# Kernel optimization log

Hardware: AMD Instinct MI355X
Metric: run time of the kernel (lower is better)

Reference implementation:

```python
import jax, jax.numpy as jnp
import numpy as np

D_MODEL = 1024
NUM_HEADS = 16
D_K = D_MODEL // NUM_HEADS
LN_EPS = 1e-5


def setup_inputs() -> dict:
    key = jax.random.key(0)
    ks = jax.random.split(key, 16)
    B, SQ, SK = 2, 2048, 2048
    s = 1.0 / np.sqrt(D_MODEL)
    inp = {
        "query": jax.random.normal(ks[0], (B, SQ, D_MODEL), jnp.float32),
        "key": jax.random.normal(ks[1], (B, SK, D_MODEL), jnp.float32),
        "value": jax.random.normal(ks[2], (B, SK, D_MODEL), jnp.float32),
        "mask": jax.random.randint(ks[3], (B, SQ, SK), 0, 2, jnp.int32),
        "w_q": jax.random.normal(ks[4], (D_MODEL, D_MODEL), jnp.float32) * s,
        "b_q": jnp.zeros((D_MODEL,), jnp.float32),
        "w_k": jax.random.normal(ks[5], (D_MODEL, D_MODEL), jnp.float32) * s,
        "b_k": jnp.zeros((D_MODEL,), jnp.float32),
        "w_v": jax.random.normal(ks[6], (D_MODEL, D_MODEL), jnp.float32) * s,
        "b_v": jnp.zeros((D_MODEL,), jnp.float32),
        "w_o": jax.random.normal(ks[7], (D_MODEL, D_MODEL), jnp.float32) * s,
        "b_o": jnp.zeros((D_MODEL,), jnp.float32),
        "ln_gamma": jnp.ones((D_MODEL,), jnp.float32),
        "ln_beta": jnp.zeros((D_MODEL,), jnp.float32),
    }
    return inp


def _split_heads(x):
    B, S, _ = x.shape
    return x.reshape(B, S, NUM_HEADS, D_K).transpose(0, 2, 1, 3)  # [B,H,S,Dk]


def reference(query, key, value, mask, w_q, b_q, w_k, b_k, w_v, b_v, w_o, b_o, ln_gamma, ln_beta):
    residual = query
    # torch Linear: y = x @ W.T + b
    Q = _split_heads(jnp.einsum('bsd,ed->bse', query, w_q) + b_q)
    K = _split_heads(jnp.einsum('bsd,ed->bse', key, w_k) + b_k)
    V = _split_heads(jnp.einsum('bsd,ed->bse', value, w_v) + b_v)
    scores = jnp.einsum('bhqd,bhkd->bhqk', Q, K) / jnp.sqrt(jnp.float32(D_K))
    scores = jnp.where(mask[:, None, :, :] == 0, jnp.float32(-1e9), scores)
    attn = jax.nn.softmax(scores, axis=-1)
    # dropout: eval mode (identity)
    ctx = jnp.einsum('bhqk,bhkd->bhqd', attn, V)
    B, H, SQ, Dk = ctx.shape
    ctx = ctx.transpose(0, 2, 1, 3).reshape(B, SQ, D_MODEL)
    out = jnp.einsum('bsd,ed->bse', ctx, w_o) + b_o + residual
    mu = jnp.mean(out, axis=-1, keepdims=True)
    var = jnp.mean(jnp.square(out - mu), axis=-1, keepdims=True)
    out = (out - mu) * jax.lax.rsqrt(var + LN_EPS) * ln_gamma + ln_beta
    return out
```

## Files before the change

kernel.cpp:

```cpp
#include <hip/hip_runtime.h>

typedef unsigned short u16;
typedef __attribute__((ext_vector_type(8))) short bf16x8;
typedef __attribute__((ext_vector_type(4))) float f32x4;

#define LOG2E 1.4426950408889634f
#define QSCALE (LOG2E / 8.0f)
#define PSTR 144

__device__ __forceinline__ u16 f2bf(float f) {
  union { float f; unsigned u; } v; v.f = f;
  unsigned r = v.u + 0x7fffu + ((v.u >> 16) & 1u);
  return (u16)(r >> 16);
}

__device__ __forceinline__ void gload_lds16(const void* g, void* l) {
  __builtin_amdgcn_global_load_lds(
      (const __attribute__((address_space(1))) unsigned int*)(unsigned long long)g,
      (__attribute__((address_space(3))) unsigned int*)(unsigned int)(unsigned long long)l,
      16, 0, 0);
}

__global__ __launch_bounds__(256) void prep_kernel(
    const float* __restrict__ q, const float* __restrict__ k, const float* __restrict__ v,
    const float* __restrict__ wq, const float* __restrict__ wk, const float* __restrict__ wv,
    const float* __restrict__ wo, const int* __restrict__ mask,
    u16* __restrict__ Xq, u16* __restrict__ Xk, u16* __restrict__ Xv,
    u16* __restrict__ Wq, u16* __restrict__ Wk, u16* __restrict__ Wv, u16* __restrict__ Wo,
    unsigned long long* __restrict__ Mp) {
  const int bx = blockIdx.x;
  if (bx < 16384) {
    const float* src; u16* dst; float sc; int idx;
    if (bx < 12288) {
      int seg = bx >> 12;
      idx = (bx & 4095) * 256 + threadIdx.x;
      src = seg == 0 ? q : (seg == 1 ? k : v);
      dst = seg == 0 ? Xq : (seg == 1 ? Xk : Xv);
      sc = 1.f;
    } else {
      int t = bx - 12288, seg = t >> 10;
      idx = (t & 1023) * 256 + threadIdx.x;
      src = seg == 0 ? wq : (seg == 1 ? wk : (seg == 2 ? wv : wo));
      dst = seg == 0 ? Wq : (seg == 1 ? Wk : (seg == 2 ? Wv : Wo));
      sc = seg == 0 ? QSCALE : 1.f;
    }
    float4 x = ((const float4*)src)[idx];
    ushort4 o;
    o.x = f2bf(x.x * sc); o.y = f2bf(x.y * sc);
    o.z = f2bf(x.z * sc); o.w = f2bf(x.w * sc);
    ((ushort4*)dst)[idx] = o;
  } else {
    int gw = (((bx - 16384) * 256) + threadIdx.x) >> 6;
    int lane = threadIdx.x & 63;
    for (int w = gw; w < 131072; w += 4096) {
      int m = mask[(size_t)w * 64 + lane];
      unsigned long long b = __ballot(m != 0);
      if (lane == 0) Mp[w] = b;
    }
  }
}

__global__ __launch_bounds__(256, 2) void gemm_kernel(
    const u16* __restrict__ Xq, const u16* __restrict__ Xk, const u16* __restrict__ Xv,
    const u16* __restrict__ Wq, const u16* __restrict__ Wk, const u16* __restrict__ Wv,
    const u16* __restrict__ Wo, const u16* __restrict__ Ctx,
    const float* __restrict__ bq, const float* __restrict__ bk, const float* __restrict__ bv,
    const float* __restrict__ bo, const float* __restrict__ resid,
    u16* __restrict__ Qd, u16* __restrict__ Kd, u16* __restrict__ Vtd, float* __restrict__ outp,
    int mode_base) {
  __shared__ __align__(16) u16 As[4096];
  __shared__ __align__(16) u16 Bs[4096];
  const int mode = mode_base + blockIdx.z;
  const int tid = threadIdx.x;
  const int wid = tid >> 6, l = tid & 63, quad = l >> 4, ln = l & 15;
  const int wm = wid >> 1, wn = wid & 1;

  const u16 *A, *B; const float* bias;
  if (mode == 0)      { A = Wq; B = Xq;  bias = bq; }
  else if (mode == 1) { A = Wk; B = Xk;  bias = bk; }
  else if (mode == 2) { A = Xv; B = Wv;  bias = bv; }
  else                { A = Wo; B = Ctx; bias = bo; }
  int mBase, nBase;
  if (mode == 2) { mBase = blockIdx.x * 128; nBase = blockIdx.y * 128; }
  else           { mBase = blockIdx.y * 128; nBase = blockIdx.x * 128; }

  const u16* Ag = A + (size_t)mBase * 1024;
  const u16* Bg = B + (size_t)nBase * 1024;

  f32x4 acc[4][4] = {};

  for (int k0 = 0; k0 < 1024; k0 += 32) {
    if (k0) __syncthreads();
    {
      int i0 = tid, i1 = tid + 256;
      gload_lds16(Ag + (size_t)(i0 & 127) * 1024 + k0 + (i0 >> 7) * 8, &As[i0 * 8]);
      gload_lds16(Ag + (size_t)(i1 & 127) * 1024 + k0 + (i1 >> 7) * 8, &As[i1 * 8]);
      gload_lds16(Bg + (size_t)(i0 & 127) * 1024 + k0 + (i0 >> 7) * 8, &Bs[i0 * 8]);
      gload_lds16(Bg + (size_t)(i1 & 127) * 1024 + k0 + (i1 >> 7) * 8, &Bs[i1 * 8]);
    }
    __syncthreads();
    bf16x8 af[4], bf[4];
#pragma unroll
    for (int i = 0; i < 4; ++i)
      af[i] = *(const bf16x8*)&As[(quad * 128 + wm * 64 + i * 16 + ln) * 8];
#pragma unroll
    for (int j = 0; j < 4; ++j)
      bf[j] = *(const bf16x8*)&Bs[(quad * 128 + wn * 64 + j * 16 + ln) * 8];
#pragma unroll
    for (int i = 0; i < 4; ++i)
#pragma unroll
      for (int j = 0; j < 4; ++j)
        acc[i][j] = __builtin_amdgcn_mfma_f32_16x16x32_bf16(af[i], bf[j], acc[i][j], 0, 0, 0);
  }

  const float bscale = (mode == 0) ? QSCALE : 1.0f;
#pragma unroll
  for (int i = 0; i < 4; ++i) {
    int m4 = mBase + wm * 64 + i * 16 + quad * 4;
#pragma unroll
    for (int j = 0; j < 4; ++j) {
      int n = nBase + wn * 64 + j * 16 + ln;
      f32x4 v = acc[i][j];
      if (mode <= 1) {
        float4 bb = *(const float4*)(bias + m4);
        int h = m4 >> 6, d = m4 & 63;
        int b = n >> 11, s = n & 2047;
        u16* dst = (mode == 0 ? Qd : Kd) + (((size_t)(b * 16 + h) * 2048 + s) * 64 + d);
        ushort4 o;
        o.x = f2bf(v[0] + bb.x * bscale); o.y = f2bf(v[1] + bb.y * bscale);
        o.z = f2bf(v[2] + bb.z * bscale); o.w = f2bf(v[3] + bb.w * bscale);
        *(ushort4*)dst = o;
      } else if (mode == 2) {
        float bb = bias[n];
        int h = n >> 6, d = n & 63;
        int b = m4 >> 11, s = m4 & 2047;
        u16* dst = Vtd + (((size_t)(b * 16 + h) * 64 + d) * 2048 + s);
        ushort4 o;
        o.x = f2bf(v[0] + bb); o.y = f2bf(v[1] + bb);
        o.z = f2bf(v[2] + bb); o.w = f2bf(v[3] + bb);
        *(ushort4*)dst = o;
      } else {
        float4 bb = *(const float4*)(bias + m4);
        float4 rr = *(const float4*)(resid + (size_t)n * 1024 + m4);
        float4 o;
        o.x = v[0] + bb.x + rr.x; o.y = v[1] + bb.y + rr.y;
        o.z = v[2] + bb.z + rr.z; o.w = v[3] + bb.w + rr.w;
        *(float4*)(outp + (size_t)n * 1024 + m4) = o;
      }
    }
  }
}

__global__ __launch_bounds__(256, 2) void attn_kernel(
    const u16* __restrict__ Qg, const u16* __restrict__ Kg, const u16* __restrict__ Vtg,
    const unsigned* __restrict__ Mp, u16* __restrict__ ctx) {
  __shared__ __align__(16) u16 UN[18432];
  __shared__ __align__(16) u16 Vs[8192];
  const int tid = threadIdx.x;
  const int wid = tid >> 6, l = tid & 63, quad = l >> 4, ln = l & 15;
  const int q4 = quad * 4;
  const int bh = blockIdx.y, b = bh >> 4, h = bh & 15;
  const int qBase = blockIdx.x * 128;
  const int wq = wid * 32;

  bf16x8 qf[2][2];
#pragma unroll
  for (int qt = 0; qt < 2; ++qt)
#pragma unroll
    for (int kc = 0; kc < 2; ++kc)
      qf[qt][kc] = *(const bf16x8*)(Qg + (((size_t)bh * 2048 + qBase + wq + qt * 16 + ln) * 64 +
                                          kc * 32 + quad * 8));

  f32x4 oacc[2][4] = {};
  f32x4 lsum[2] = {};
  const bf16x8 vone = {(short)0x3F80, (short)0x3F80, (short)0x3F80, (short)0x3F80,
                       (short)0x3F80, (short)0x3F80, (short)0x3F80, (short)0x3F80};

  const unsigned* mrow[2];
  mrow[0] = Mp + ((size_t)b * 2048 + qBase + wq + ln) * 64;
  mrow[1] = mrow[0] + 16 * 64;

  for (int it = 0; it < 16; ++it) {
    const int kvB = it * 128;
    __syncthreads();
#pragma unroll
    for (int r = 0; r < 4; ++r) {
      int c = r * 256 + tid;
      gload_lds16(Kg + (((size_t)bh * 2048 + kvB + (c & 127)) * 64 + (c >> 7) * 8), &UN[c * 8]);
    }
#pragma unroll
    for (int r = 0; r < 4; ++r) {
      int c = r * 256 + tid;
      gload_lds16(Vtg + (((size_t)bh * 64 + (c & 63)) * 2048 + kvB + (c >> 6) * 8), &Vs[c * 8]);
    }
    __syncthreads();

    f32x4 s[8][2];
#pragma unroll
    for (int mt = 0; mt < 8; ++mt) {
      bf16x8 k0 = *(const bf16x8*)&UN[((0 + quad) * 128 + mt * 16 + ln) * 8];
      bf16x8 k1 = *(const bf16x8*)&UN[((4 + quad) * 128 + mt * 16 + ln) * 8];
#pragma unroll
      for (int qt = 0; qt < 2; ++qt) {
        f32x4 z = {0.f, 0.f, 0.f, 0.f};
        z = __builtin_amdgcn_mfma_f32_16x16x32_bf16(k0, qf[qt][0], z, 0, 0, 0);
        s[mt][qt] = __builtin_amdgcn_mfma_f32_16x16x32_bf16(k1, qf[qt][1], z, 0, 0, 0);
      }
    }

    unsigned ww[2][4];
    {
      uint4 m0 = *(const uint4*)(mrow[0] + it * 4);
      uint4 m1 = *(const uint4*)(mrow[1] + it * 4);
      ww[0][0] = m0.x; ww[0][1] = m0.y; ww[0][2] = m0.z; ww[0][3] = m0.w;
      ww[1][0] = m1.x; ww[1][1] = m1.y; ww[1][2] = m1.z; ww[1][3] = m1.w;
    }
    uint2 pk[8][2];
#pragma unroll
    for (int qt = 0; qt < 2; ++qt)
#pragma unroll
      for (int mt = 0; mt < 8; ++mt) {
        unsigned nib = (ww[qt][mt >> 1] >> ((mt & 1) * 16 + q4)) & 0xFu;
        float p0 = __builtin_amdgcn_exp2f((nib & 1u) ? s[mt][qt][0] : -1e30f);
        float p1 = __builtin_amdgcn_exp2f((nib & 2u) ? s[mt][qt][1] : -1e30f);
        float p2 = __builtin_amdgcn_exp2f((nib & 4u) ? s[mt][qt][2] : -1e30f);
        float p3 = __builtin_amdgcn_exp2f((nib & 8u) ? s[mt][qt][3] : -1e30f);
        pk[mt][qt].x = __builtin_amdgcn_perm(__float_as_uint(p1) + 0x8000u,
                                             __float_as_uint(p0) + 0x8000u, 0x07060302u);
        pk[mt][qt].y = __builtin_amdgcn_perm(__float_as_uint(p3) + 0x8000u,
                                             __float_as_uint(p2) + 0x8000u, 0x07060302u);
      }

    __syncthreads();
#pragma unroll
    for (int qt = 0; qt < 2; ++qt) {
      int qrow = wq + qt * 16 + ln;
#pragma unroll
      for (int mt = 0; mt < 8; ++mt)
        *(uint2*)&UN[qrow * PSTR + mt * 16 + q4] = pk[mt][qt];
    }
    __syncthreads();

#pragma unroll
    for (int kc2 = 0; kc2 < 4; ++kc2) {
      bf16x8 aP[2];
#pragma unroll
      for (int qt = 0; qt < 2; ++qt)
        aP[qt] = *(const bf16x8*)&UN[(wq + qt * 16 + ln) * PSTR + kc2 * 32 + quad * 8];
#pragma unroll
      for (int nt = 0; nt < 4; ++nt) {
        bf16x8 bV = *(const bf16x8*)&Vs[((kc2 * 4 + quad) * 64 + nt * 16 + ln) * 8];
#pragma unroll
        for (int qt = 0; qt < 2; ++qt)
          oacc[qt][nt] = __builtin_amdgcn_mfma_f32_16x16x32_bf16(aP[qt], bV, oacc[qt][nt], 0, 0, 0);
      }
#pragma unroll
      for (int qt = 0; qt < 2; ++qt)
        lsum[qt] = __builtin_amdgcn_mfma_f32_16x16x32_bf16(aP[qt], vone, lsum[qt], 0, 0, 0);
    }
  }

  __syncthreads();
#pragma unroll
  for (int qt = 0; qt < 2; ++qt)
#pragma unroll
    for (int r = 0; r < 4; ++r) {
      float il = 1.0f / lsum[qt][r];
      int q = wq + qt * 16 + q4 + r;
#pragma unroll
      for (int nt = 0; nt < 4; ++nt)
        UN[q * 64 + nt * 16 + ln] = f2bf(oacc[qt][nt][r] * il);
    }
  __syncthreads();
#pragma unroll
  for (int r = 0; r < 4; ++r) {
    int c = r * 256 + tid;
    int q = c >> 3, ch = c & 7;
    *(uint4*)(ctx + ((size_t)(b * 2048 + qBase + q) * 1024 + h * 64 + ch * 8)) =
        *(const uint4*)&UN[q * 64 + ch * 8];
  }
}

__global__ __launch_bounds__(256) void ln_kernel(const float* __restrict__ x,
                                                 const float* __restrict__ gamma,
                                                 const float* __restrict__ beta,
                                                 float* __restrict__ out) {
  __shared__ float red[8];
  const int tid = threadIdx.x;
  const size_t row = blockIdx.x;
  const float4 v = ((const float4*)(x + row * 1024))[tid];
  float s1 = v.x + v.y + v.z + v.w;
  float s2 = v.x * v.x + v.y * v.y + v.z * v.z + v.w * v.w;
#pragma unroll
  for (int o = 32; o >= 1; o >>= 1) {
    s1 += __shfl_xor(s1, o);
    s2 += __shfl_xor(s2, o);
  }
  if ((tid & 63) == 0) { red[(tid >> 6) * 2] = s1; red[(tid >> 6) * 2 + 1] = s2; }
  __syncthreads();
  s1 = red[0] + red[2] + red[4] + red[6];
  s2 = red[1] + red[3] + red[5] + red[7];
  float mu = s1 * (1.f / 1024.f);
  float var = s2 * (1.f / 1024.f) - mu * mu;
  float inv = rsqrtf(var + 1e-5f);
  float4 g = ((const float4*)gamma)[tid];
  float4 be = ((const float4*)beta)[tid];
  float4 o;
  o.x = (v.x - mu) * inv * g.x + be.x;
  o.y = (v.y - mu) * inv * g.y + be.y;
  o.z = (v.z - mu) * inv * g.z + be.z;
  o.w = (v.w - mu) * inv * g.w + be.w;
  ((float4*)(out + row * 1024))[tid] = o;
}

extern "C" void kernel_launch(void* const* d_in, const int* in_sizes, int n_in,
                              void* d_out, int out_size, void* d_ws, size_t ws_size,
                              hipStream_t stream) {
  const float* query = (const float*)d_in[0];
  const float* key   = (const float*)d_in[1];
  const float* value = (const float*)d_in[2];
  const int*   mask  = (const int*)d_in[3];
  const float* w_q = (const float*)d_in[4];
  const float* b_q = (const float*)d_in[5];
  const float* w_k = (const float*)d_in[6];
  const float* b_k = (const float*)d_in[7];
  const float* w_v = (const float*)d_in[8];
  const float* b_v = (const float*)d_in[9];
  const float* w_o = (const float*)d_in[10];
  const float* b_o = (const float*)d_in[11];
  const float* ln_g = (const float*)d_in[12];
  const float* ln_b = (const float*)d_in[13];
  float* out = (float*)d_out;

  char* ws = (char*)d_ws;
  u16* Xq = (u16*)(ws + ((size_t)0 << 20));
  u16* Xk = (u16*)(ws + ((size_t)8 << 20));
  u16* Xv = (u16*)(ws + ((size_t)16 << 20));
  float* outpre = (float*)(ws + ((size_t)8 << 20));
  u16* Wq = (u16*)(ws + ((size_t)24 << 20));
  u16* Wk = (u16*)(ws + ((size_t)26 << 20));
  u16* Wv = (u16*)(ws + ((size_t)28 << 20));
  u16* Wo = (u16*)(ws + ((size_t)30 << 20));
  u16* Qd = (u16*)(ws + ((size_t)32 << 20));
  u16* Kd = (u16*)(ws + ((size_t)40 << 20));
  u16* Vtd = (u16*)(ws + ((size_t)48 << 20));
  unsigned long long* Mp = (unsigned long long*)(ws + ((size_t)56 << 20));
  u16* ctx = Xq;

  prep_kernel<<<17408, 256, 0, stream>>>(query, key, value, w_q, w_k, w_v, w_o, mask,
                                         Xq, Xk, Xv, Wq, Wk, Wv, Wo, Mp);
  gemm_kernel<<<dim3(32, 8, 3), 256, 0, stream>>>(Xq, Xk, Xv, Wq, Wk, Wv, Wo, ctx,
      b_q, b_k, b_v, b_o, query, Qd, Kd, Vtd, outpre, 0);
  attn_kernel<<<dim3(16, 32), 256, 0, stream>>>(Qd, Kd, Vtd, (const unsigned*)Mp, ctx);
  gemm_kernel<<<dim3(32, 8, 1), 256, 0, stream>>>(Xq, Xk, Xv, Wq, Wk, Wv, Wo, ctx,
      b_q, b_k, b_v, b_o, query, Qd, Kd, Vtd, outpre, 3);
  ln_kernel<<<4096, 256, 0, stream>>>(outpre, ln_g, ln_b, out);
}
```

Measured before the change: 351.8 us.

## Stage GEMM epilogues through LDS for coalesced stores; move residual/bias add into LayerNorm

The GEMM epilogue now writes each accumulator tile into shared memory (padded stride) and then issues 16-byte coalesced global stores for the Q/K, transposed V, and output-projection results, instead of scattered 8-byte stores. The residual and output bias add moves from the output-projection GEMM into the LayerNorm kernel, which now reads the residual directly. The mask-packing part of prep_kernel gets more blocks, so each wave handles fewer iterations. In exchange, the GEMM uses a larger shared buffer, which may reduce occupancy, and adds extra barriers.

```diff
diff --git a/kernel.cpp b/kernel.cpp
--- a/kernel.cpp
+++ b/kernel.cpp
@@ -52,7 +52,7 @@
   } else {
     int gw = (((bx - 16384) * 256) + threadIdx.x) >> 6;
     int lane = threadIdx.x & 63;
-    for (int w = gw; w < 131072; w += 4096) {
+    for (int w = gw; w < 131072; w += 16384) {
       int m = mask[(size_t)w * 64 + lane];
       unsigned long long b = __ballot(m != 0);
       if (lane == 0) Mp[w] = b;
@@ -65,11 +65,11 @@
     const u16* __restrict__ Wq, const u16* __restrict__ Wk, const u16* __restrict__ Wv,
     const u16* __restrict__ Wo, const u16* __restrict__ Ctx,
     const float* __restrict__ bq, const float* __restrict__ bk, const float* __restrict__ bv,
-    const float* __restrict__ bo, const float* __restrict__ resid,
     u16* __restrict__ Qd, u16* __restrict__ Kd, u16* __restrict__ Vtd, float* __restrict__ outp,
     int mode_base) {
-  __shared__ __align__(16) u16 As[4096];
-  __shared__ __align__(16) u16 Bs[4096];
+  __shared__ __align__(16) u16 SH[17408];
+  u16* As = SH;
+  u16* Bs = SH + 4096;
   const int mode = mode_base + blockIdx.z;
   const int tid = threadIdx.x;
   const int wid = tid >> 6, l = tid & 63, quad = l >> 4, ln = l & 15;
@@ -79,7 +79,7 @@
   if (mode == 0)      { A = Wq; B = Xq;  bias = bq; }
   else if (mode == 1) { A = Wk; B = Xk;  bias = bk; }
   else if (mode == 2) { A = Xv; B = Wv;  bias = bv; }
-  else                { A = Wo; B = Ctx; bias = bo; }
+  else                { A = Wo; B = Ctx; bias = bq; }
   int mBase, nBase;
   if (mode == 2) { mBase = blockIdx.x * 128; nBase = blockIdx.y * 128; }
   else           { mBase = blockIdx.y * 128; nBase = blockIdx.x * 128; }
@@ -113,39 +113,86 @@
         acc[i][j] = __builtin_amdgcn_mfma_f32_16x16x32_bf16(af[i], bf[j], acc[i][j], 0, 0, 0);
   }
 
-  const float bscale = (mode == 0) ? QSCALE : 1.0f;
-#pragma unroll
-  for (int i = 0; i < 4; ++i) {
-    int m4 = mBase + wm * 64 + i * 16 + quad * 4;
-#pragma unroll
-    for (int j = 0; j < 4; ++j) {
-      int n = nBase + wn * 64 + j * 16 + ln;
-      f32x4 v = acc[i][j];
-      if (mode <= 1) {
-        float4 bb = *(const float4*)(bias + m4);
-        int h = m4 >> 6, d = m4 & 63;
-        int b = n >> 11, s = n & 2047;
-        u16* dst = (mode == 0 ? Qd : Kd) + (((size_t)(b * 16 + h) * 2048 + s) * 64 + d);
+  __syncthreads();
+
+  if (mode <= 1) {
+    const float bscale = (mode == 0) ? QSCALE : 1.0f;
+#pragma unroll
+    for (int i = 0; i < 4; ++i) {
+      int f0 = wm * 64 + i * 16 + quad * 4;
+      float4 bb = *(const float4*)(bias + mBase + f0);
+#pragma unroll
+      for (int j = 0; j < 4; ++j) {
+        int sl = wn * 64 + j * 16 + ln;
+        f32x4 v = acc[i][j];
         ushort4 o;
         o.x = f2bf(v[0] + bb.x * bscale); o.y = f2bf(v[1] + bb.y * bscale);
         o.z = f2bf(v[2] + bb.z * bscale); o.w = f2bf(v[3] + bb.w * bscale);
-        *(ushort4*)dst = o;
-      } else if (mode == 2) {
-        float bb = bias[n];
-        int h = n >> 6, d = n & 63;
-        int b = m4 >> 11, s = m4 & 2047;
-        u16* dst = Vtd + (((size_t)(b * 16 + h) * 64 + d) * 2048 + s);
+        *(ushort4*)&SH[sl * 136 + f0] = o;
+      }
+    }
+    __syncthreads();
+    u16* dstQK = (mode == 0) ? Qd : Kd;
+#pragma unroll
+    for (int p = 0; p < 8; ++p) {
+      int sl = p * 16 + (tid >> 4);
+      int fl = (tid & 15) * 8;
+      uint4 w = *(const uint4*)&SH[sl * 136 + fl];
+      int s = nBase + sl, f = mBase + fl;
+      int h = f >> 6, d = f & 63, b = s >> 11, sr = s & 2047;
+      *(uint4*)(dstQK + (((size_t)(b * 16 + h) * 2048 + sr) * 64 + d)) = w;
+    }
+  } else if (mode == 2) {
+#pragma unroll
+    for (int j = 0; j < 4; ++j) {
+      int fl = wn * 64 + j * 16 + ln;
+      float bb = bias[nBase + fl];
+#pragma unroll
+      for (int i = 0; i < 4; ++i) {
+        int s0 = wm * 64 + i * 16 + quad * 4;
+        f32x4 v = acc[i][j];
         ushort4 o;
         o.x = f2bf(v[0] + bb); o.y = f2bf(v[1] + bb);
         o.z = f2bf(v[2] + bb); o.w = f2bf(v[3] + bb);
-        *(ushort4*)dst = o;
-      } else {
-        float4 bb = *(const float4*)(bias + m4);
-        float4 rr = *(const float4*)(resid + (size_t)n * 1024 + m4);
-        float4 o;
-        o.x = v[0] + bb.x + rr.x; o.y = v[1] + bb.y + rr.y;
-        o.z = v[2] + bb.z + rr.z; o.w = v[3] + bb.w + rr.w;
-        *(float4*)(outp + (size_t)n * 1024 + m4) = o;
+        *(ushort4*)&SH[fl * 136 + s0] = o;
+      }
+    }
+    __syncthreads();
+#pragma unroll
+    for (int p = 0; p < 8; ++p) {
+      int fl = p * 16 + (tid >> 4);
+      int sl = (tid & 15) * 8;
+      uint4 w = *(const uint4*)&SH[fl * 136 + sl];
+      int f = nBase + fl, s = mBase + sl;
+      int h = f >> 6, d = f & 63, b = s >> 11, sr = s & 2047;
+      *(uint4*)(Vtd + (((size_t)(b * 16 + h) * 64 + d) * 2048 + sr)) = w;
+    }
+  } else {
+    float* ES = (float*)SH;
+#pragma unroll
+    for (int h2 = 0; h2 < 2; ++h2) {
+      if (h2) __syncthreads();
+      if (wn == h2) {
+#pragma unroll
+        for (int i = 0; i < 4; ++i) {
+          int f0 = wm * 64 + i * 16 + quad * 4;
+#pragma unroll
+          for (int j = 0; j < 4; ++j) {
+            int sl = j * 16 + ln;
+            f32x4 v = acc[i][j];
+            float4 o; o.x = v[0]; o.y = v[1]; o.z = v[2]; o.w = v[3];
+            *(float4*)&ES[sl * 132 + f0] = o;
+          }
+        }
+      }
+      __syncthreads();
+#pragma unroll
+      for (int p = 0; p < 8; ++p) {
+        int sl = p * 8 + (tid >> 5);
+        int fl = (tid & 31) * 4;
+        float4 w = *(const float4*)&ES[sl * 132 + fl];
+        int s = nBase + h2 * 64 + sl;
+        *(float4*)(outp + (size_t)s * 1024 + mBase + fl) = w;
       }
     }
   }
@@ -282,13 +329,18 @@
 }
 
 __global__ __launch_bounds__(256) void ln_kernel(const float* __restrict__ x,
+                                                 const float* __restrict__ resid,
+                                                 const float* __restrict__ bo,
                                                  const float* __restrict__ gamma,
                                                  const float* __restrict__ beta,
                                                  float* __restrict__ out) {
   __shared__ float red[8];
   const int tid = threadIdx.x;
   const size_t row = blockIdx.x;
-  const float4 v = ((const float4*)(x + row * 1024))[tid];
+  float4 v = ((const float4*)(x + row * 1024))[tid];
+  const float4 rr = ((const float4*)(resid + row * 1024))[tid];
+  const float4 bb = ((const float4*)bo)[tid];
+  v.x += rr.x + bb.x; v.y += rr.y + bb.y; v.z += rr.z + bb.z; v.w += rr.w + bb.w;
   float s1 = v.x + v.y + v.z + v.w;
   float s2 = v.x * v.x + v.y * v.y + v.z * v.z + v.w * v.w;
 #pragma unroll
@@ -347,12 +399,12 @@
   unsigned long long* Mp = (unsigned long long*)(ws + ((size_t)56 << 20));
   u16* ctx = Xq;
 
-  prep_kernel<<<17408, 256, 0, stream>>>(query, key, value, w_q, w_k, w_v, w_o, mask,
+  prep_kernel<<<20480, 256, 0, stream>>>(query, key, value, w_q, w_k, w_v, w_o, mask,
                                          Xq, Xk, Xv, Wq, Wk, Wv, Wo, Mp);
   gemm_kernel<<<dim3(32, 8, 3), 256, 0, stream>>>(Xq, Xk, Xv, Wq, Wk, Wv, Wo, ctx,
-      b_q, b_k, b_v, b_o, query, Qd, Kd, Vtd, outpre, 0);
+      b_q, b_k, b_v, Qd, Kd, Vtd, outpre, 0);
   attn_kernel<<<dim3(16, 32), 256, 0, stream>>>(Qd, Kd, Vtd, (const unsigned*)Mp, ctx);
   gemm_kernel<<<dim3(32, 8, 1), 256, 0, stream>>>(Xq, Xk, Xv, Wq, Wk, Wv, Wo, ctx,
-      b_q, b_k, b_v, b_o, query, Qd, Kd, Vtd, outpre, 3);
-  ln_kernel<<<4096, 256, 0, stream>>>(outpre, ln_g, ln_b, out);
-}
+      b_q, b_k, b_v, Qd, Kd, Vtd, outpre, 3);
+  ln_kernel<<<4096, 256, 0, stream>>>(outpre, query, b_o, ln_g, ln_b, out);
+}
```

New measurement: 332.5 us. 1.06x faster.
